# Optimization experiments

Hardware: AMD Instinct MI355X
Metric: run time of the kernel (lower is better)

The kernel has to match this reference:

```python
import jax, jax.numpy as jnp
import numpy as np

NEAR, FAR = 0.05, 6.0
STEPSIZE = 0.5
ALPHA_INIT = 1e-6
XYZ_MIN = np.array([-1.0, -1.0, -1.0], np.float32)
XYZ_MAX = np.array([1.0, 1.0, 1.0], np.float32)
WORLD = (160, 160, 160)
VOXEL_SIZE = 2.0 / 160.0  # ((prod span)/num_voxels)^(1/3)
N_SAMPLES = int(np.linalg.norm(np.array(WORLD) + 1) / STEPSIZE) + 1  # 558
ACT_SHIFT = float(np.log(1.0 / (1.0 - ALPHA_INIT) - 1.0))


def setup_inputs() -> dict:
    key = jax.random.key(0)
    k1, k2, k3, k4, k5, k6, k7 = jax.random.split(key, 7)
    rays_o = (jax.random.uniform(k1, (8192, 3), jnp.float32) - 0.5) * 1.2  # inside bbox
    rd = jax.random.normal(k2, (8192, 3), jnp.float32)
    rays_d = rd / jnp.linalg.norm(rd, axis=-1, keepdims=True)
    jitter = jax.random.uniform(k3, (8192, 1), jnp.float32)
    em_modes = jax.random.randint(k4, (8192,), 0, 2, jnp.int32)
    density = jax.random.normal(k5, (1, 160, 160, 160), jnp.float32) * 0.1
    off_color = jax.random.normal(k6, (3, 160, 160, 160), jnp.float32) * 0.1
    emo_color = jax.random.normal(k7, (3, 160, 160, 160), jnp.float32) * 0.1
    return {"rays_o": rays_o, "rays_d": rays_d, "jitter": jitter, "em_modes": em_modes,
            "density": density, "off_color": off_color, "emo_color": emo_color}


def grid_sampler(pts, grid):
    """Trilinear interp, align_corners=True, zero padding. grid [C,Nx,Ny,Nz], pts [...,3] -> [...,C]."""
    C = grid.shape[0]
    sizes = np.array(grid.shape[1:], np.int32)
    lead = pts.shape[:-1]
    t = (pts.reshape(-1, 3) - XYZ_MIN) / (XYZ_MAX - XYZ_MIN)
    idx = t * (jnp.asarray(sizes, pts.dtype) - 1)  # voxel-space coords
    i0 = jnp.floor(idx).astype(jnp.int32)
    f = idx - i0.astype(pts.dtype)
    out = jnp.zeros((i0.shape[0], C), grid.dtype)
    for corner in range(8):
        off = np.array([(corner >> 2) & 1, (corner >> 1) & 1, corner & 1], np.int32)
        ci = i0 + off  # [N,3]
        w = jnp.prod(jnp.where(off[None, :] == 1, f, 1.0 - f), axis=-1)  # [N]
        valid = jnp.all((ci >= 0) & (ci < sizes[None, :]), axis=-1)
        cc = jnp.clip(ci, 0, sizes[None, :] - 1)
        vals = grid[:, cc[:, 0], cc[:, 1], cc[:, 2]].T  # [N,C]
        out = out + (w * valid)[:, None] * vals
    return out.reshape(*lead, C)


def sample_ray(rays_o, rays_d, jitter):
    vec = jnp.where(rays_d == 0, 1e-6, rays_d)
    rate_a = (XYZ_MAX - rays_o) / vec
    rate_b = (XYZ_MIN - rays_o) / vec
    t_min = jnp.clip(jnp.minimum(rate_a, rate_b).max(-1), NEAR, FAR)
    t_max = jnp.clip(jnp.maximum(rate_a, rate_b).min(-1), NEAR, FAR)
    mask_out = t_max <= t_min  # [R]
    rng = jnp.arange(N_SAMPLES, dtype=rays_o.dtype)[None, :] + jitter  # [R,S]
    step = STEPSIZE * VOXEL_SIZE * rng
    interpx = t_min[:, None] + step / jnp.linalg.norm(rays_d, axis=-1, keepdims=True)
    rays_pts = rays_o[:, None, :] + rays_d[:, None, :] * interpx[..., None]  # [R,S,3]
    mask_out = mask_out[:, None] | ((rays_pts < XYZ_MIN) | (rays_pts > XYZ_MAX)).any(-1)
    return rays_pts, mask_out


def reference(rays_o, rays_d, jitter, em_modes, density, off_color, emo_color):
    rays_pts, mask_out = sample_ray(rays_o, rays_d, jitter)
    dens = grid_sampler(rays_pts, density)[..., 0]  # [R,S]
    alpha_all = 1.0 - jnp.exp(-jax.nn.softplus(dens + ACT_SHIFT) * STEPSIZE)
    alpha = jnp.where(mask_out, 0.0, alpha_all)
    p = jnp.clip(1.0 - alpha, 1e-10, None)
    alphainv_cum = jnp.concatenate([jnp.ones_like(p[..., :1]), jnp.cumprod(p, -1)], -1)  # [R,S+1]
    weights = alpha * alphainv_cum[..., :-1]
    on_mask = (em_modes == 1)[:, None, None]
    emo = jax.nn.sigmoid(grid_sampler(rays_pts, emo_color))
    off = jax.nn.sigmoid(grid_sampler(rays_pts, off_color))
    rgb = jnp.where(on_mask, emo, 0.0) + off  # [R,S,3]
    rgb_marched = (weights[..., None] * rgb).sum(-2)  # [R,3]
    return (alphainv_cum, weights, alphainv_cum[..., -1:], rgb, rgb_marched)
```

## Files before the change

### kernel.cpp

```cpp
#include <hip/hip_runtime.h>
#include <math.h>


namespace {
constexpr int   kR   = 8192;
constexpr int   kS   = 558;
constexpr int   kG   = 160;
constexpr int   kG2  = kG * kG;
constexpr int   kG3  = kG * kG * kG;
constexpr float kNear = 0.05f;
constexpr float kFar  = 6.0f;
constexpr float kStepWorld = 0.5f * (2.0f / 160.0f);
constexpr float kActShift = -13.815509557963774f;
constexpr float kLog2e = 1.4426950408889634f;
}

typedef unsigned int nuint4 __attribute__((ext_vector_type(4)));

__device__ __forceinline__ float fexp(float x) {
  return __builtin_amdgcn_exp2f(x * kLog2e);
}
__device__ __forceinline__ float sigmoidf_(float x) {
  return __builtin_amdgcn_rcpf(1.0f + fexp(-x));
}
__device__ __forceinline__ float bf_lo(unsigned int u) {
  union { unsigned int i; float f; } x; x.i = u << 16; return x.f;
}
__device__ __forceinline__ float bf_hi(unsigned int u) {
  union { unsigned int i; float f; } x; x.i = u; return x.f;
}
__device__ __forceinline__ unsigned int f2bf(float f) {
  union { float f; unsigned int i; } x; x.f = f;
  unsigned int lsb = (x.i >> 16) & 1u;
  return (x.i + 0x7fffu + lsb) >> 16;
}

__global__ __launch_bounds__(256) void repack_grids(
    const float* __restrict__ density,
    const float* __restrict__ off_c,
    const float* __restrict__ emo_c,
    nuint4* __restrict__ packed)
{
  const int v = blockIdx.x * blockDim.x + threadIdx.x;
  if (v >= kG3) return;
  const float d  = __builtin_nontemporal_load(density + v);
  const float f0 = __builtin_nontemporal_load(off_c + v);
  const float f1 = __builtin_nontemporal_load(off_c + v + kG3);
  const float f2 = __builtin_nontemporal_load(off_c + v + 2 * kG3);
  const float e0 = __builtin_nontemporal_load(emo_c + v);
  const float e1 = __builtin_nontemporal_load(emo_c + v + kG3);
  const float e2 = __builtin_nontemporal_load(emo_c + v + 2 * kG3);
  nuint4 q;
  q.x = f2bf(d)  | (f2bf(f0) << 16);
  q.y = f2bf(f1) | (f2bf(f2) << 16);
  q.z = f2bf(e0) | (f2bf(e1) << 16);
  q.w = f2bf(e2);
  __builtin_nontemporal_store(q, packed + v);
}

__global__ __launch_bounds__(256) void dvgo_fwd(
    const float* __restrict__ rays_o,
    const float* __restrict__ rays_d,
    const float* __restrict__ jitter,
    const int*   __restrict__ em_modes,
    const uint4* __restrict__ packed4,
    const uint2* __restrict__ packed2,
    float* __restrict__ out)
{
  const int tid  = blockIdx.x * blockDim.x + threadIdx.x;
  const int ray  = tid >> 6;
  const int lane = tid & 63;
  if (ray >= kR) return;

  const float ox = rays_o[ray * 3 + 0];
  const float oy = rays_o[ray * 3 + 1];
  const float oz = rays_o[ray * 3 + 2];
  const float dx = rays_d[ray * 3 + 0];
  const float dy = rays_d[ray * 3 + 1];
  const float dz = rays_d[ray * 3 + 2];
  const float jit = jitter[ray];
  const bool  on  = (em_modes[ray] == 1);

  const float vx = (dx == 0.0f) ? 1e-6f : dx;
  const float vy = (dy == 0.0f) ? 1e-6f : dy;
  const float vz = (dz == 0.0f) ? 1e-6f : dz;
  const float ivx = __builtin_amdgcn_rcpf(vx);
  const float ivy = __builtin_amdgcn_rcpf(vy);
  const float ivz = __builtin_amdgcn_rcpf(vz);
  const float rax = ( 1.0f - ox) * ivx, rbx = (-1.0f - ox) * ivx;
  const float ray_a = ( 1.0f - oy) * ivy, rby = (-1.0f - oy) * ivy;
  const float raz = ( 1.0f - oz) * ivz, rbz = (-1.0f - oz) * ivz;
  float tmin = fmaxf(fmaxf(fminf(rax, rbx), fminf(ray_a, rby)), fminf(raz, rbz));
  float tmax = fminf(fminf(fmaxf(rax, rbx), fmaxf(ray_a, rby)), fmaxf(raz, rbz));
  tmin = fminf(fmaxf(tmin, kNear), kFar);
  tmax = fminf(fmaxf(tmax, kNear), kFar);
  const bool  ray_out = (tmax <= tmin);
  const float stepc = kStepWorld *
      __builtin_amdgcn_rsqf(dx * dx + dy * dy + dz * dz);

  float* out_ainv = out;
  float* out_w    = out + (size_t)kR * (kS + 1);
  float* out_last = out_w + (size_t)kR * kS;
  float* out_rgb  = out_last + kR;
  float* out_rm   = out_rgb + (size_t)kR * kS * 3;

  if (lane == 0)
    __builtin_nontemporal_store(1.0f, out_ainv + (size_t)ray * (kS + 1));

  const float c_base = on ? 1.0f : 0.5f;

  float carry = 1.0f;
  float accr = 0.0f, accg = 0.0f, accb = 0.0f;
  bool dead = false;

  #pragma unroll 1
  for (int chunk = 0; chunk < (kS + 63) / 64; ++chunk) {
    const int  s      = chunk * 64 + lane;
    const bool active = (s < kS);

    if (!dead) {
      const float t  = tmin + stepc * ((float)s + jit);
      const float px = fmaf(dx, t, ox);
      const float py = fmaf(dy, t, oy);
      const float pz = fmaf(dz, t, oz);
      const bool inb = (px >= -1.0f) & (px <= 1.0f) &
                       (py >= -1.0f) & (py <= 1.0f) &
                       (pz >= -1.0f) & (pz <= 1.0f);
      const bool masked = ray_out || !inb;

      const float fx = (px + 1.0f) * 0.5f * (float)(kG - 1);
      const float fy = (py + 1.0f) * 0.5f * (float)(kG - 1);
      const float fz = (pz + 1.0f) * 0.5f * (float)(kG - 1);
      const int ix = (int)floorf(fx);
      const int iy = (int)floorf(fy);
      const int iz = (int)floorf(fz);

      const bool reach = active &&
          (ix >= -1) && (ix <= kG - 1) &&
          (iy >= -1) && (iy <= kG - 1) &&
          (iz >= -1) && (iz <= kG - 1);
      if (__ballot(reach) == 0ull) {
        dead = true;
      } else {
        const float wx = fx - (float)ix;
        const float wy = fy - (float)iy;
        const float wz = fz - (float)iz;
        const float x0 = 1.0f - wx, y0 = 1.0f - wy, z0 = 1.0f - wz;
        const float wxy00 = x0 * y0, wxy01 = x0 * wy;
        const float wxy10 = wx * y0, wxy11 = wx * wy;
        float w8[8];
        w8[0] = wxy00 * z0; w8[1] = wxy00 * wz;
        w8[2] = wxy01 * z0; w8[3] = wxy01 * wz;
        w8[4] = wxy10 * z0; w8[5] = wxy10 * wz;
        w8[6] = wxy11 * z0; w8[7] = wxy11 * wz;

        float dsum = 0.0f;
        float o0 = 0.0f, o1 = 0.0f, o2 = 0.0f;
        float e0 = 0.0f, e1 = 0.0f, e2 = 0.0f;

        const bool interior = active &&
            (ix >= 0) && (ix < kG - 1) &&
            (iy >= 0) && (iy < kG - 1) &&
            (iz >= 0) && (iz < kG - 1);

        if (interior) {
          const int base = (ix * kG + iy) * kG + iz;
          if (on) {
            #pragma unroll
            for (int c = 0; c < 8; ++c) {
              const int gi = base + ((c >> 2) & 1) * kG2 + ((c >> 1) & 1) * kG + (c & 1);
              const float w = w8[c];
              const uint4 q = packed4[gi];
              dsum = fmaf(w, bf_lo(q.x), dsum);
              o0   = fmaf(w, bf_hi(q.x), o0);
              o1   = fmaf(w, bf_lo(q.y), o1);
              o2   = fmaf(w, bf_hi(q.y), o2);
              e0   = fmaf(w, bf_lo(q.z), e0);
              e1   = fmaf(w, bf_hi(q.z), e1);
              e2   = fmaf(w, bf_lo(q.w), e2);
            }
          } else {
            #pragma unroll
            for (int c = 0; c < 8; ++c) {
              const int gi = base + ((c >> 2) & 1) * kG2 + ((c >> 1) & 1) * kG + (c & 1);
              const float w = w8[c];
              const uint2 qa = packed2[(size_t)gi * 2];
              dsum = fmaf(w, bf_lo(qa.x), dsum);
              o0   = fmaf(w, bf_hi(qa.x), o0);
              o1   = fmaf(w, bf_lo(qa.y), o1);
              o2   = fmaf(w, bf_hi(qa.y), o2);
            }
          }
        } else if (reach) {
          #pragma unroll
          for (int c = 0; c < 8; ++c) {
            const int cx = ix + ((c >> 2) & 1);
            const int cy = iy + ((c >> 1) & 1);
            const int cz = iz + (c & 1);
            const bool valid = ((unsigned)cx < (unsigned)kG) &
                               ((unsigned)cy < (unsigned)kG) &
                               ((unsigned)cz < (unsigned)kG);
            const float wv = valid ? w8[c] : 0.0f;
            const int gx = min(max(cx, 0), kG - 1);
            const int gy = min(max(cy, 0), kG - 1);
            const int gz = min(max(cz, 0), kG - 1);
            const int gi = (gx * kG + gy) * kG + gz;
            const uint2 qa = packed2[(size_t)gi * 2];
            dsum = fmaf(wv, bf_lo(qa.x), dsum);
            o0   = fmaf(wv, bf_hi(qa.x), o0);
            o1   = fmaf(wv, bf_lo(qa.y), o1);
            o2   = fmaf(wv, bf_hi(qa.y), o2);
            if (on) {
              const uint2 qb = packed2[(size_t)gi * 2 + 1];
              e0 = fmaf(wv, bf_lo(qb.x), e0);
              e1 = fmaf(wv, bf_hi(qb.x), e1);
              e2 = fmaf(wv, bf_lo(qb.y), e2);
            }
          }
        }

        float p = 1.0f;
        if (active && !masked) {
          const float ex = fexp(dsum + kActShift);
          p = fmaxf(__builtin_amdgcn_rsqf(1.0f + ex), 1e-10f);
        }
        const float alpha = 1.0f - p;

        float incl = p;
        #pragma unroll
        for (int o = 1; o < 64; o <<= 1) {
          const float n = __shfl_up(incl, o, 64);
          if (lane >= o) incl *= n;
        }
        float excl = __shfl_up(incl, 1, 64);
        if (lane == 0) excl = 1.0f;
        const float ainv_prev = carry * excl;
        const float ainv_next = carry * incl;
        const float wgt = alpha * ainv_prev;
        carry *= __shfl(incl, 63, 64);

        float rr = sigmoidf_(o0);
        float gg = sigmoidf_(o1);
        float bb = sigmoidf_(o2);
        if (on) {
          rr += sigmoidf_(e0);
          gg += sigmoidf_(e1);
          bb += sigmoidf_(e2);
        }

        if (active) {
          __builtin_nontemporal_store(ainv_next,
              out_ainv + (size_t)ray * (kS + 1) + s + 1);
          __builtin_nontemporal_store(wgt, out_w + (size_t)ray * kS + s);
          const size_t rb = ((size_t)ray * kS + s) * 3;
          __builtin_nontemporal_store(rr, out_rgb + rb + 0);
          __builtin_nontemporal_store(gg, out_rgb + rb + 1);
          __builtin_nontemporal_store(bb, out_rgb + rb + 2);
          accr = fmaf(wgt, rr, accr);
          accg = fmaf(wgt, gg, accg);
          accb = fmaf(wgt, bb, accb);
        }
        continue;
      }
    }

    if (active) {
      __builtin_nontemporal_store(carry,
          out_ainv + (size_t)ray * (kS + 1) + s + 1);
      __builtin_nontemporal_store(0.0f, out_w + (size_t)ray * kS + s);
      const size_t rb = ((size_t)ray * kS + s) * 3;
      __builtin_nontemporal_store(c_base, out_rgb + rb + 0);
      __builtin_nontemporal_store(c_base, out_rgb + rb + 1);
      __builtin_nontemporal_store(c_base, out_rgb + rb + 2);
    }
  }

  #pragma unroll
  for (int o = 32; o > 0; o >>= 1) {
    accr += __shfl_xor(accr, o, 64);
    accg += __shfl_xor(accg, o, 64);
    accb += __shfl_xor(accb, o, 64);
  }
  if (lane == 0) {
    out_last[ray] = carry;
    out_rm[(size_t)ray * 3 + 0] = accr;
    out_rm[(size_t)ray * 3 + 1] = accg;
    out_rm[(size_t)ray * 3 + 2] = accb;
  }
}

extern "C" void kernel_launch(void* const* d_in, const int* in_sizes, int n_in,
                              void* d_out, int out_size, void* d_ws, size_t ws_size,
                              hipStream_t stream) {
  const float* rays_o  = (const float*)d_in[0];
  const float* rays_d  = (const float*)d_in[1];
  const float* jitter  = (const float*)d_in[2];
  const int*   em      = (const int*)d_in[3];
  const float* density = (const float*)d_in[4];
  const float* off_c   = (const float*)d_in[5];
  const float* emo_c   = (const float*)d_in[6];
  float* out = (float*)d_out;

  nuint4* packed = (nuint4*)d_ws;
  (void)ws_size;

  hipLaunchKernelGGL(repack_grids, dim3((kG3 + 255) / 256), dim3(256), 0,
                     stream, density, off_c, emo_c, packed);

  const int threads = 256;
  const int blocks  = (kR * 64) / threads;
  hipLaunchKernelGGL(dvgo_fwd, dim3(blocks), dim3(threads), 0, stream,
                     rays_o, rays_d, jitter, em, (const uint4*)packed,
                     (const uint2*)packed, out);
}
```

Baseline: 239.7 us.

## Split ray marching into parallel per-chunk sampling kernel and separate scan kernel

The single fused kernel, where each wave walked its ray's sample chunks serially, is replaced by two kernels. The first runs one wave per (ray, chunk), doing the trilinear gathers, writing transmittance factors to a workspace buffer, writing rgb, and recording whether each chunk is live. The second kernel performs the per-ray cumulative-product scan, writes weights, and rereads rgb to accumulate the marched color. The aim is to expose much more memory-level parallelism for the latency-bound gathers, at the cost of extra global traffic for the p buffer and the rgb reread, plus larger workspace use.

```diff
diff --git a/kernel.cpp b/kernel.cpp
--- a/kernel.cpp
+++ b/kernel.cpp
@@ -5,6 +5,7 @@
 namespace {
 constexpr int   kR   = 8192;
 constexpr int   kS   = 558;
+constexpr int   kNC  = (kS + 63) / 64;
 constexpr int   kG   = 160;
 constexpr int   kG2  = kG * kG;
 constexpr int   kG3  = kG * kG * kG;
@@ -13,6 +14,7 @@
 constexpr float kStepWorld = 0.5f * (2.0f / 160.0f);
 constexpr float kActShift = -13.815509557963774f;
 constexpr float kLog2e = 1.4426950408889634f;
+constexpr size_t kPackedBytes = (size_t)kG3 * 16;
 }
 
 typedef unsigned int nuint4 __attribute__((ext_vector_type(4)));
@@ -58,18 +60,22 @@
   __builtin_nontemporal_store(q, packed + v);
 }
 
-__global__ __launch_bounds__(256) void dvgo_fwd(
+__global__ __launch_bounds__(256) void dvgo_sample(
     const float* __restrict__ rays_o,
     const float* __restrict__ rays_d,
     const float* __restrict__ jitter,
     const int*   __restrict__ em_modes,
     const uint4* __restrict__ packed4,
     const uint2* __restrict__ packed2,
+    float* __restrict__ p_buf,
+    int*   __restrict__ live_flags,
     float* __restrict__ out)
 {
-  const int tid  = blockIdx.x * blockDim.x + threadIdx.x;
-  const int ray  = tid >> 6;
-  const int lane = tid & 63;
+  const int tid   = blockIdx.x * blockDim.x + threadIdx.x;
+  const int wid   = tid >> 6;
+  const int lane  = tid & 63;
+  const int ray   = wid / kNC;
+  const int chunk = wid - ray * kNC;
   if (ray >= kR) return;
 
   const float ox = rays_o[ray * 3 + 0];
@@ -98,180 +104,217 @@
   const float stepc = kStepWorld *
       __builtin_amdgcn_rsqf(dx * dx + dy * dy + dz * dz);
 
+  const int  s      = chunk * 64 + lane;
+  const bool active = (s < kS);
+
+  const float t  = tmin + stepc * ((float)s + jit);
+  const float px = fmaf(dx, t, ox);
+  const float py = fmaf(dy, t, oy);
+  const float pz = fmaf(dz, t, oz);
+  const bool inb = (px >= -1.0f) & (px <= 1.0f) &
+                   (py >= -1.0f) & (py <= 1.0f) &
+                   (pz >= -1.0f) & (pz <= 1.0f);
+  const bool masked = ray_out || !inb;
+
+  const float fx = (px + 1.0f) * 0.5f * (float)(kG - 1);
+  const float fy = (py + 1.0f) * 0.5f * (float)(kG - 1);
+  const float fz = (pz + 1.0f) * 0.5f * (float)(kG - 1);
+  const int ix = (int)floorf(fx);
+  const int iy = (int)floorf(fy);
+  const int iz = (int)floorf(fz);
+
+  const bool reach = active &&
+      (ix >= -1) && (ix <= kG - 1) &&
+      (iy >= -1) && (iy <= kG - 1) &&
+      (iz >= -1) && (iz <= kG - 1);
+  const unsigned long long live = __ballot(reach);
+  if (lane == 0) live_flags[ray * kNC + chunk] = (live != 0ull) ? 1 : 0;
+
+  float* out_rgb = out + (size_t)kR * (kS + 1) + (size_t)kR * kS + kR;
+  const float c_base = on ? 1.0f : 0.5f;
+
+  if (live == 0ull) {
+    if (active) {
+      const size_t rb = ((size_t)ray * kS + s) * 3;
+      __builtin_nontemporal_store(c_base, out_rgb + rb + 0);
+      __builtin_nontemporal_store(c_base, out_rgb + rb + 1);
+      __builtin_nontemporal_store(c_base, out_rgb + rb + 2);
+    }
+    return;
+  }
+
+  const float wx = fx - (float)ix;
+  const float wy = fy - (float)iy;
+  const float wz = fz - (float)iz;
+  const float x0 = 1.0f - wx, y0 = 1.0f - wy, z0 = 1.0f - wz;
+  const float wxy00 = x0 * y0, wxy01 = x0 * wy;
+  const float wxy10 = wx * y0, wxy11 = wx * wy;
+  float w8[8];
+  w8[0] = wxy00 * z0; w8[1] = wxy00 * wz;
+  w8[2] = wxy01 * z0; w8[3] = wxy01 * wz;
+  w8[4] = wxy10 * z0; w8[5] = wxy10 * wz;
+  w8[6] = wxy11 * z0; w8[7] = wxy11 * wz;
+
+  float dsum = 0.0f;
+  float o0 = 0.0f, o1 = 0.0f, o2 = 0.0f;
+  float e0 = 0.0f, e1 = 0.0f, e2 = 0.0f;
+
+  const bool interior = active &&
+      (ix >= 0) && (ix < kG - 1) &&
+      (iy >= 0) && (iy < kG - 1) &&
+      (iz >= 0) && (iz < kG - 1);
+
+  if (interior) {
+    const int base = (ix * kG + iy) * kG + iz;
+    if (on) {
+      #pragma unroll
+      for (int c = 0; c < 8; ++c) {
+        const int gi = base + ((c >> 2) & 1) * kG2 + ((c >> 1) & 1) * kG + (c & 1);
+        const float w = w8[c];
+        const uint4 q = packed4[gi];
+        dsum = fmaf(w, bf_lo(q.x), dsum);
+        o0   = fmaf(w, bf_hi(q.x), o0);
+        o1   = fmaf(w, bf_lo(q.y), o1);
+        o2   = fmaf(w, bf_hi(q.y), o2);
+        e0   = fmaf(w, bf_lo(q.z), e0);
+        e1   = fmaf(w, bf_hi(q.z), e1);
+        e2   = fmaf(w, bf_lo(q.w), e2);
+      }
+    } else {
+      #pragma unroll
+      for (int c = 0; c < 8; ++c) {
+        const int gi = base + ((c >> 2) & 1) * kG2 + ((c >> 1) & 1) * kG + (c & 1);
+        const float w = w8[c];
+        const uint2 qa = packed2[(size_t)gi * 2];
+        dsum = fmaf(w, bf_lo(qa.x), dsum);
+        o0   = fmaf(w, bf_hi(qa.x), o0);
+        o1   = fmaf(w, bf_lo(qa.y), o1);
+        o2   = fmaf(w, bf_hi(qa.y), o2);
+      }
+    }
+  } else if (reach) {
+    #pragma unroll
+    for (int c = 0; c < 8; ++c) {
+      const int cx = ix + ((c >> 2) & 1);
+      const int cy = iy + ((c >> 1) & 1);
+      const int cz = iz + (c & 1);
+      const bool valid = ((unsigned)cx < (unsigned)kG) &
+                         ((unsigned)cy < (unsigned)kG) &
+                         ((unsigned)cz < (unsigned)kG);
+      const float wv = valid ? w8[c] : 0.0f;
+      const int gx = min(max(cx, 0), kG - 1);
+      const int gy = min(max(cy, 0), kG - 1);
+      const int gz = min(max(cz, 0), kG - 1);
+      const int gi = (gx * kG + gy) * kG + gz;
+      const uint2 qa = packed2[(size_t)gi * 2];
+      dsum = fmaf(wv, bf_lo(qa.x), dsum);
+      o0   = fmaf(wv, bf_hi(qa.x), o0);
+      o1   = fmaf(wv, bf_lo(qa.y), o1);
+      o2   = fmaf(wv, bf_hi(qa.y), o2);
+      if (on) {
+        const uint2 qb = packed2[(size_t)gi * 2 + 1];
+        e0 = fmaf(wv, bf_lo(qb.x), e0);
+        e1 = fmaf(wv, bf_hi(qb.x), e1);
+        e2 = fmaf(wv, bf_lo(qb.y), e2);
+      }
+    }
+  }
+
+  float p = 1.0f;
+  if (active && !masked) {
+    const float ex = fexp(dsum + kActShift);
+    p = fmaxf(__builtin_amdgcn_rsqf(1.0f + ex), 1e-10f);
+  }
+
+  float rr = sigmoidf_(o0);
+  float gg = sigmoidf_(o1);
+  float bb = sigmoidf_(o2);
+  if (on) {
+    rr += sigmoidf_(e0);
+    gg += sigmoidf_(e1);
+    bb += sigmoidf_(e2);
+  }
+
+  if (active) {
+    p_buf[(size_t)ray * kS + s] = p;
+    const size_t rb = ((size_t)ray * kS + s) * 3;
+    __builtin_nontemporal_store(rr, out_rgb + rb + 0);
+    __builtin_nontemporal_store(gg, out_rgb + rb + 1);
+    __builtin_nontemporal_store(bb, out_rgb + rb + 2);
+  }
+}
+
+__global__ __launch_bounds__(256) void dvgo_scan(
+    const float* __restrict__ p_buf,
+    const int*   __restrict__ live_flags,
+    float* __restrict__ out)
+{
+  const int tid  = blockIdx.x * blockDim.x + threadIdx.x;
+  const int ray  = tid >> 6;
+  const int lane = tid & 63;
+  if (ray >= kR) return;
+
   float* out_ainv = out;
   float* out_w    = out + (size_t)kR * (kS + 1);
   float* out_last = out_w + (size_t)kR * kS;
   float* out_rgb  = out_last + kR;
   float* out_rm   = out_rgb + (size_t)kR * kS * 3;
 
+  const int fl = (lane < kNC) ? live_flags[ray * kNC + lane] : 0;
+  const unsigned long long fmask = __ballot(fl != 0);
+
   if (lane == 0)
     __builtin_nontemporal_store(1.0f, out_ainv + (size_t)ray * (kS + 1));
 
-  const float c_base = on ? 1.0f : 0.5f;
+  float pv[kNC];
+  #pragma unroll
+  for (int c = 0; c < kNC; ++c) {
+    const int s = c * 64 + lane;
+    const bool use = (s < kS) && ((fmask >> c) & 1ull);
+    pv[c] = use ? p_buf[(size_t)ray * kS + s] : 1.0f;
+  }
 
   float carry = 1.0f;
   float accr = 0.0f, accg = 0.0f, accb = 0.0f;
-  bool dead = false;
-
-  #pragma unroll 1
-  for (int chunk = 0; chunk < (kS + 63) / 64; ++chunk) {
+
+  #pragma unroll
+  for (int chunk = 0; chunk < kNC; ++chunk) {
     const int  s      = chunk * 64 + lane;
     const bool active = (s < kS);
 
-    if (!dead) {
-      const float t  = tmin + stepc * ((float)s + jit);
-      const float px = fmaf(dx, t, ox);
-      const float py = fmaf(dy, t, oy);
-      const float pz = fmaf(dz, t, oz);
-      const bool inb = (px >= -1.0f) & (px <= 1.0f) &
-                       (py >= -1.0f) & (py <= 1.0f) &
-                       (pz >= -1.0f) & (pz <= 1.0f);
-      const bool masked = ray_out || !inb;
-
-      const float fx = (px + 1.0f) * 0.5f * (float)(kG - 1);
-      const float fy = (py + 1.0f) * 0.5f * (float)(kG - 1);
-      const float fz = (pz + 1.0f) * 0.5f * (float)(kG - 1);
-      const int ix = (int)floorf(fx);
-      const int iy = (int)floorf(fy);
-      const int iz = (int)floorf(fz);
-
-      const bool reach = active &&
-          (ix >= -1) && (ix <= kG - 1) &&
-          (iy >= -1) && (iy <= kG - 1) &&
-          (iz >= -1) && (iz <= kG - 1);
-      if (__ballot(reach) == 0ull) {
-        dead = true;
-      } else {
-        const float wx = fx - (float)ix;
-        const float wy = fy - (float)iy;
-        const float wz = fz - (float)iz;
-        const float x0 = 1.0f - wx, y0 = 1.0f - wy, z0 = 1.0f - wz;
-        const float wxy00 = x0 * y0, wxy01 = x0 * wy;
-        const float wxy10 = wx * y0, wxy11 = wx * wy;
-        float w8[8];
-        w8[0] = wxy00 * z0; w8[1] = wxy00 * wz;
-        w8[2] = wxy01 * z0; w8[3] = wxy01 * wz;
-        w8[4] = wxy10 * z0; w8[5] = wxy10 * wz;
-        w8[6] = wxy11 * z0; w8[7] = wxy11 * wz;
-
-        float dsum = 0.0f;
-        float o0 = 0.0f, o1 = 0.0f, o2 = 0.0f;
-        float e0 = 0.0f, e1 = 0.0f, e2 = 0.0f;
-
-        const bool interior = active &&
-            (ix >= 0) && (ix < kG - 1) &&
-            (iy >= 0) && (iy < kG - 1) &&
-            (iz >= 0) && (iz < kG - 1);
-
-        if (interior) {
-          const int base = (ix * kG + iy) * kG + iz;
-          if (on) {
-            #pragma unroll
-            for (int c = 0; c < 8; ++c) {
-              const int gi = base + ((c >> 2) & 1) * kG2 + ((c >> 1) & 1) * kG + (c & 1);
-              const float w = w8[c];
-              const uint4 q = packed4[gi];
-              dsum = fmaf(w, bf_lo(q.x), dsum);
-              o0   = fmaf(w, bf_hi(q.x), o0);
-              o1   = fmaf(w, bf_lo(q.y), o1);
-              o2   = fmaf(w, bf_hi(q.y), o2);
-              e0   = fmaf(w, bf_lo(q.z), e0);
-              e1   = fmaf(w, bf_hi(q.z), e1);
-              e2   = fmaf(w, bf_lo(q.w), e2);
-            }
-          } else {
-            #pragma unroll
-            for (int c = 0; c < 8; ++c) {
-              const int gi = base + ((c >> 2) & 1) * kG2 + ((c >> 1) & 1) * kG + (c & 1);
-              const float w = w8[c];
-              const uint2 qa = packed2[(size_t)gi * 2];
-              dsum = fmaf(w, bf_lo(qa.x), dsum);
-              o0   = fmaf(w, bf_hi(qa.x), o0);
-              o1   = fmaf(w, bf_lo(qa.y), o1);
-              o2   = fmaf(w, bf_hi(qa.y), o2);
-            }
-          }
-        } else if (reach) {
-          #pragma unroll
-          for (int c = 0; c < 8; ++c) {
-            const int cx = ix + ((c >> 2) & 1);
-            const int cy = iy + ((c >> 1) & 1);
-            const int cz = iz + (c & 1);
-            const bool valid = ((unsigned)cx < (unsigned)kG) &
-                               ((unsigned)cy < (unsigned)kG) &
-                               ((unsigned)cz < (unsigned)kG);
-            const float wv = valid ? w8[c] : 0.0f;
-            const int gx = min(max(cx, 0), kG - 1);
-            const int gy = min(max(cy, 0), kG - 1);
-            const int gz = min(max(cz, 0), kG - 1);
-            const int gi = (gx * kG + gy) * kG + gz;
-            const uint2 qa = packed2[(size_t)gi * 2];
-            dsum = fmaf(wv, bf_lo(qa.x), dsum);
-            o0   = fmaf(wv, bf_hi(qa.x), o0);
-            o1   = fmaf(wv, bf_lo(qa.y), o1);
-            o2   = fmaf(wv, bf_hi(qa.y), o2);
-            if (on) {
-              const uint2 qb = packed2[(size_t)gi * 2 + 1];
-              e0 = fmaf(wv, bf_lo(qb.x), e0);
-              e1 = fmaf(wv, bf_hi(qb.x), e1);
-              e2 = fmaf(wv, bf_lo(qb.y), e2);
-            }
-          }
-        }
-
-        float p = 1.0f;
-        if (active && !masked) {
-          const float ex = fexp(dsum + kActShift);
-          p = fmaxf(__builtin_amdgcn_rsqf(1.0f + ex), 1e-10f);
-        }
-        const float alpha = 1.0f - p;
-
-        float incl = p;
-        #pragma unroll
-        for (int o = 1; o < 64; o <<= 1) {
-          const float n = __shfl_up(incl, o, 64);
-          if (lane >= o) incl *= n;
-        }
-        float excl = __shfl_up(incl, 1, 64);
-        if (lane == 0) excl = 1.0f;
-        const float ainv_prev = carry * excl;
-        const float ainv_next = carry * incl;
-        const float wgt = alpha * ainv_prev;
-        carry *= __shfl(incl, 63, 64);
-
-        float rr = sigmoidf_(o0);
-        float gg = sigmoidf_(o1);
-        float bb = sigmoidf_(o2);
-        if (on) {
-          rr += sigmoidf_(e0);
-          gg += sigmoidf_(e1);
-          bb += sigmoidf_(e2);
-        }
-
-        if (active) {
-          __builtin_nontemporal_store(ainv_next,
-              out_ainv + (size_t)ray * (kS + 1) + s + 1);
-          __builtin_nontemporal_store(wgt, out_w + (size_t)ray * kS + s);
-          const size_t rb = ((size_t)ray * kS + s) * 3;
-          __builtin_nontemporal_store(rr, out_rgb + rb + 0);
-          __builtin_nontemporal_store(gg, out_rgb + rb + 1);
-          __builtin_nontemporal_store(bb, out_rgb + rb + 2);
-          accr = fmaf(wgt, rr, accr);
-          accg = fmaf(wgt, gg, accg);
-          accb = fmaf(wgt, bb, accb);
-        }
-        continue;
-      }
-    }
-
-    if (active) {
-      __builtin_nontemporal_store(carry,
-          out_ainv + (size_t)ray * (kS + 1) + s + 1);
-      __builtin_nontemporal_store(0.0f, out_w + (size_t)ray * kS + s);
-      const size_t rb = ((size_t)ray * kS + s) * 3;
-      __builtin_nontemporal_store(c_base, out_rgb + rb + 0);
-      __builtin_nontemporal_store(c_base, out_rgb + rb + 1);
-      __builtin_nontemporal_store(c_base, out_rgb + rb + 2);
+    if ((fmask >> chunk) & 1ull) {
+      const float p = pv[chunk];
+      float incl = p;
+      #pragma unroll
+      for (int o = 1; o < 64; o <<= 1) {
+        const float n = __shfl_up(incl, o, 64);
+        if (lane >= o) incl *= n;
+      }
+      float excl = __shfl_up(incl, 1, 64);
+      if (lane == 0) excl = 1.0f;
+      const float ainv_prev = carry * excl;
+      const float ainv_next = carry * incl;
+      const float wgt = (1.0f - p) * ainv_prev;
+      carry *= __shfl(incl, 63, 64);
+
+      if (active) {
+        __builtin_nontemporal_store(ainv_next,
+            out_ainv + (size_t)ray * (kS + 1) + s + 1);
+        __builtin_nontemporal_store(wgt, out_w + (size_t)ray * kS + s);
+        const size_t rb = ((size_t)ray * kS + s) * 3;
+        const float rr = __builtin_nontemporal_load(out_rgb + rb + 0);
+        const float gg = __builtin_nontemporal_load(out_rgb + rb + 1);
+        const float bb = __builtin_nontemporal_load(out_rgb + rb + 2);
+        accr = fmaf(wgt, rr, accr);
+        accg = fmaf(wgt, gg, accg);
+        accb = fmaf(wgt, bb, accb);
+      }
+    } else {
+      if (active) {
+        __builtin_nontemporal_store(carry,
+            out_ainv + (size_t)ray * (kS + 1) + s + 1);
+        __builtin_nontemporal_store(0.0f, out_w + (size_t)ray * kS + s);
+      }
     }
   }
 
@@ -301,15 +344,22 @@
   const float* emo_c   = (const float*)d_in[6];
   float* out = (float*)d_out;
 
-  nuint4* packed = (nuint4*)d_ws;
+  char* ws = (char*)d_ws;
+  nuint4* packed  = (nuint4*)ws;
+  float*  p_buf   = (float*)(ws + kPackedBytes);
+  int*    flags   = (int*)(p_buf + (size_t)kR * kS);
   (void)ws_size;
 
   hipLaunchKernelGGL(repack_grids, dim3((kG3 + 255) / 256), dim3(256), 0,
                      stream, density, off_c, emo_c, packed);
 
-  const int threads = 256;
-  const int blocks  = (kR * 64) / threads;
-  hipLaunchKernelGGL(dvgo_fwd, dim3(blocks), dim3(threads), 0, stream,
+  const int waves_a  = kR * kNC;
+  const int blocks_a = waves_a / 4;
+  hipLaunchKernelGGL(dvgo_sample, dim3(blocks_a), dim3(256), 0, stream,
                      rays_o, rays_d, jitter, em, (const uint4*)packed,
-                     (const uint2*)packed, out);
-}
+                     (const uint2*)packed, p_buf, flags, out);
+
+  const int blocks_b = (kR * 64) / 256;
+  hipLaunchKernelGGL(dvgo_scan, dim3(blocks_b), dim3(256), 0, stream,
+                     p_buf, flags, out);
+}
```

New measurement: 260.0 us. +8.5%, slower.
